# Kernel optimization log

Hardware: AMD Instinct MI355X
Metric: run time of the kernel (lower is better)

The kernel has to match this reference:

```python
import jax, jax.numpy as jnp
import numpy as np

EPS = 1e-5
K = 2  # superpatch hop


def _bn(x, gamma, beta, mean, var):
    # inference-mode BatchNorm2d over channel dim (NCHW)
    inv = gamma / jnp.sqrt(var + EPS)
    return x * inv[None, :, None, None] + (beta - mean * inv)[None, :, None, None]


def _conv1x1(x, w, b):
    # x: [B,C,H,W], w: [O,C], b: [O]
    return jnp.einsum('bchw,oc->bohw', x, w) + b[None, :, None, None]


def setup_inputs() -> dict:
    key = jax.random.key(0)
    ks = jax.random.split(key, 24)
    B, C, H, W = 32, 192, 56, 56
    r = lambda k, shape, s=0.05: jax.random.normal(k, shape, dtype=jnp.float32) * s
    pv = lambda k, shape: jax.random.uniform(k, shape, dtype=jnp.float32, minval=0.5, maxval=1.5)
    inp = {
        'x': jax.random.normal(ks[0], (B, C, H, W), dtype=jnp.float32),
        # RepCPE: depthwise 7x7 conv, groups=C -> weight [C,1,7,7]
        'cpe_w': r(ks[1], (C, 1, 7, 7)),
        'cpe_b': r(ks[2], (C,)),
        # fc1: 1x1 conv C->C + BN
        'fc1_w': r(ks[3], (C, C)), 'fc1_b': r(ks[4], (C,)),
        'bn1_g': pv(ks[5], (C,)), 'bn1_b': r(ks[6], (C,)),
        'bn1_m': r(ks[7], (C,), 0.1), 'bn1_v': pv(ks[8], (C,)),
        # graph_conv.nn: 1x1 conv 2C->C + BN + GELU
        'gc_w': r(ks[9], (C, 2 * C)), 'gc_b': r(ks[10], (C,)),
        'bng_g': pv(ks[11], (C,)), 'bng_b': r(ks[12], (C,)),
        'bng_m': r(ks[13], (C,), 0.1), 'bng_v': pv(ks[14], (C,)),
        # fc2: 1x1 conv C->C + BN
        'fc2_w': r(ks[15], (C, C)), 'fc2_b': r(ks[16], (C,)),
        'bn2_g': pv(ks[17], (C,)), 'bn2_b': r(ks[18], (C,)),
        'bn2_m': r(ks[19], (C,), 0.1), 'bn2_v': pv(ks[20], (C,)),
    }
    return inp


def reference(x, cpe_w, cpe_b, fc1_w, fc1_b, bn1_g, bn1_b, bn1_m, bn1_v,
              gc_w, gc_b, bng_g, bng_b, bng_m, bng_v,
              fc2_w, fc2_b, bn2_g, bn2_b, bn2_m, bn2_v):
    C = x.shape[1]
    # --- RepCPE: depthwise 7x7 conv + bias, residual add ---
    pe = jax.lax.conv_general_dilated(
        x, cpe_w, window_strides=(1, 1), padding='SAME',
        feature_group_count=C,
        dimension_numbers=('NCHW', 'OIHW', 'NCHW'))
    x = pe + cpe_b[None, :, None, None] + x
    # --- fc1: 1x1 conv + BN ---
    x = _bn(_conv1x1(x, fc1_w, fc1_b), bn1_g, bn1_b, bn1_m, bn1_v)
    # --- MRConv4d: max-relative over 4 shifted neighbor views ---
    # torch.cat([x[..., -K:, :], x[..., :-K, :]], dim=2) == roll(+K) along H, etc.
    d = jnp.maximum(jnp.roll(x, K, axis=2) - x, jnp.roll(x, -K, axis=2) - x)
    d = jnp.maximum(d, jnp.roll(x, K, axis=3) - x)
    x_j = jnp.maximum(jnp.maximum(d, jnp.roll(x, -K, axis=3) - x), 0.0)  # x_j init = x - x = 0
    xc = jnp.concatenate([x, x_j], axis=1)  # [B,2C,H,W]
    x = jax.nn.gelu(_bn(_conv1x1(xc, gc_w, gc_b), bng_g, bng_b, bng_m, bng_v),
                    approximate=False)
    # --- fc2: 1x1 conv + BN ---
    x = _bn(_conv1x1(x, fc2_w, fc2_b), bn2_g, bn2_b, bn2_m, bn2_v)
    return x
```

## Files before the change

kernel.cpp:

```cpp
#include <hip/hip_runtime.h>
#include <hip/hip_bf16.h>


#define CC   192
#define HW   3136
#define NB   32

using short8 = __attribute__((ext_vector_type(8))) short;
using f32x4  = __attribute__((ext_vector_type(4))) float;

__device__ __forceinline__ float bf2f(short s) {
  union { unsigned u; float f; } x; x.u = ((unsigned)(unsigned short)s) << 16; return x.f;
}
__device__ __forceinline__ short f2bf(float f) {
  __hip_bfloat16 h = __float2bfloat16(f);
  return *reinterpret_cast<short*>(&h);
}
__device__ __forceinline__ float geluf(float v) {
  return 0.5f * v * (1.0f + erff(v * 0.70710678118654752f));
}
__device__ __forceinline__ void gl2lds(const char* g, char* l) {
  __builtin_amdgcn_global_load_lds(
      (const __attribute__((address_space(1))) void*)g,
      (__attribute__((address_space(3))) void*)l, 16, 0, 0);
}

__global__ void __launch_bounds__(256) fold_kernel(
    const float* __restrict__ fc1_w, const float* __restrict__ fc1_b,
    const float* __restrict__ bn1_g, const float* __restrict__ bn1_b,
    const float* __restrict__ bn1_m, const float* __restrict__ bn1_v,
    const float* __restrict__ gc_w,  const float* __restrict__ gc_b,
    const float* __restrict__ bng_g, const float* __restrict__ bng_b,
    const float* __restrict__ bng_m, const float* __restrict__ bng_v,
    const float* __restrict__ fc2_w, const float* __restrict__ fc2_b,
    const float* __restrict__ bn2_g, const float* __restrict__ bn2_b,
    const float* __restrict__ bn2_m, const float* __restrict__ bn2_v,
    __hip_bfloat16* __restrict__ W1f, __hip_bfloat16* __restrict__ Wgf, __hip_bfloat16* __restrict__ W2f,
    float* __restrict__ b1f, float* __restrict__ bgf, float* __restrict__ b2f) {
  int gt = blockIdx.x * 256 + threadIdx.x;
  if (gt < 3 * CC) {
    int which = gt / CC, o = gt - which * CC;
    const float *G, *Bt, *M, *V, *Bi; float* dst;
    if (which == 0)      { G = bn1_g; Bt = bn1_b; M = bn1_m; V = bn1_v; Bi = fc1_b; dst = b1f; }
    else if (which == 1) { G = bng_g; Bt = bng_b; M = bng_m; V = bng_v; Bi = gc_b;  dst = bgf; }
    else                 { G = bn2_g; Bt = bn2_b; M = bn2_m; V = bn2_v; Bi = fc2_b; dst = b2f; }
    float inv = G[o] * rsqrtf(V[o] + 1e-5f);
    dst[o] = Bi[o] * inv + Bt[o] - M[o] * inv;
  }
  int i = gt;
  if (i < CC * CC) {
    int o = i / CC;
    float inv = bn1_g[o] * rsqrtf(bn1_v[o] + 1e-5f);
    W1f[i] = __float2bfloat16(fc1_w[i] * inv);
  } else if (i < CC * CC + CC * 2 * CC) {
    int j = i - CC * CC; int o = j / (2 * CC);
    float inv = bng_g[o] * rsqrtf(bng_v[o] + 1e-5f);
    Wgf[j] = __float2bfloat16(gc_w[j] * inv);
  } else if (i < CC * CC * 4) {
    int j = i - CC * CC * 3; int o = j / CC;
    float inv = bn2_g[o] * rsqrtf(bn2_v[o] + 1e-5f);
    W2f[j] = __float2bfloat16(fc2_w[j] * inv);
  }
}

#define CSTR 956
__global__ void __launch_bounds__(256, 4) dwconv_kernel(
    const float* __restrict__ x, const float* __restrict__ cw,
    const float* __restrict__ cb, __hip_bfloat16* __restrict__ y0pm) {
  __shared__ short in_t[16 * CSTR];
  const int t = threadIdx.x;
  int bb = blockIdx.x;
  const int rs = bb % 7;  bb /= 7;
  const int cg = bb % 12; bb /= 12;
  const int b  = bb;
  const int h0 = rs * 8;

  for (int i = t; i < 16 * CSTR / 8; i += 256) ((int4*)in_t)[i] = int4{0, 0, 0, 0};
  __syncthreads();

  for (int it = t; it < 16 * 14 * 14; it += 256) {
    int w4 = it % 14, rr = (it / 14) % 14, c = it / 196;
    int gh = h0 - 3 + rr;
    if (gh >= 0 && gh < 56) {
      float4 v = *(const float4*)(x + ((size_t)(b * CC + cg * 16 + c) * 56 + gh) * 56 + w4 * 4);
      short4 s4 = { f2bf(v.x), f2bf(v.y), f2bf(v.z), f2bf(v.w) };
      *(short4*)(in_t + c * CSTR + rr * 68 + 4 + w4 * 4) = s4;
    }
  }
  __syncthreads();

  const int c = t & 15, g = t >> 4;
  const int cgx = g % 7, rh = g / 7;
  if (g < 14) {
    const float* wp = cw + (cg * 16 + c) * 49;
    const float bias = cb[cg * 16 + c];
    const short* base = in_t + c * CSTR + rh * 4 * 68 + cgx * 8;
    float acc[4][8] = {};
    float wr[7], wn[7];
#pragma unroll
    for (int i = 0; i < 7; ++i) wr[i] = wp[i];
#pragma unroll
    for (int kh = 0; kh < 7; ++kh) {
      if (kh < 6) {
#pragma unroll
        for (int i = 0; i < 7; ++i) wn[i] = wp[(kh + 1) * 7 + i];
      }
      if (kh == 3) wr[3] += 1.0f;
#pragma unroll
      for (int r = 0; r < 4; ++r) {
        const short* rp = base + (r + kh) * 68;
        int2 q0 = *(const int2*)(rp);
        int2 q1 = *(const int2*)(rp + 4);
        int2 q2 = *(const int2*)(rp + 8);
        int2 q3 = *(const int2*)(rp + 12);
        int dw[8] = { q0.x, q0.y, q1.x, q1.y, q2.x, q2.y, q3.x, q3.y };
        float v[16];
#pragma unroll
        for (int q = 0; q < 8; ++q) {
          union { int i; float f; } lo, hi;
          lo.i = dw[q] << 16; hi.i = dw[q] & 0xffff0000;
          v[q * 2] = lo.f; v[q * 2 + 1] = hi.f;
        }
#pragma unroll
        for (int kw = 0; kw < 7; ++kw) {
          float wv = wr[kw];
#pragma unroll
          for (int ww = 0; ww < 8; ++ww)
            acc[r][ww] = fmaf(wv, v[ww + kw + 1], acc[r][ww]);
        }
      }
#pragma unroll
      for (int i = 0; i < 7; ++i) wr[i] = wn[i];
    }
    short* dst = (short*)y0pm + ((size_t)b * HW + (size_t)(h0 + rh * 4) * 56 + cgx * 8) * CC
                 + cg * 16 + c;
#pragma unroll
    for (int r = 0; r < 4; ++r)
#pragma unroll
      for (int ww = 0; ww < 8; ++ww)
        dst[(size_t)(r * 56 + ww) * CC] = f2bf(acc[r][ww] + bias);
  }
}

__device__ __forceinline__ void stage_xj(char* dst, const short* y1b, int hwbase, int t) {
#pragma unroll 2
  for (int j = 0; j < 6; ++j) {
    int idx = j * 4096 + t * 16;
    int p = idx / 384, qd = idx - p * 384;
    int co = qd >> 1;
    int hwl = hwbase + p;
    int h = hwl / 56, w = hwl - h * 56;
    int hp = (h >= 54) ? h - 54 : h + 2;
    int hm = (h < 2) ? h + 54 : h - 2;
    int wp_ = (w >= 54) ? w - 54 : w + 2;
    int wm_ = (w < 2) ? w + 54 : w - 2;
    short8 c0 = *(const short8*)(y1b + (size_t)hwl * CC + co);
    short8 n1 = *(const short8*)(y1b + (size_t)(hp * 56 + w) * CC + co);
    short8 n2 = *(const short8*)(y1b + (size_t)(hm * 56 + w) * CC + co);
    short8 n3 = *(const short8*)(y1b + (size_t)(h * 56 + wp_) * CC + co);
    short8 n4 = *(const short8*)(y1b + (size_t)(h * 56 + wm_) * CC + co);
    short8 res;
#pragma unroll
    for (int q = 0; q < 8; ++q) {
      float m = fmaxf(fmaxf(bf2f(n1[q]), bf2f(n2[q])), fmaxf(bf2f(n3[q]), bf2f(n4[q])));
      res[q] = f2bf(fmaxf(m - bf2f(c0[q]), 0.0f));
    }
    *(short8*)(dst + p * 384 + (qd ^ ((p & 7) << 4))) = res;
  }
}

template<int NCHUNK, int MODE, int MINW>
__global__ void __launch_bounds__(256, MINW) gemm_kernel(
    const __hip_bfloat16* __restrict__ actA, const __hip_bfloat16* __restrict__ actB,
    const __hip_bfloat16* __restrict__ Wf, const float* __restrict__ bfv,
    void* __restrict__ outp) {
  __shared__ char smem[2][24576];
  const int t = threadIdx.x;
  const int lane = t & 63, w = t >> 6;
  const int lrow = lane & 15, lhi = lane >> 4;
  constexpr int K_IN = NCHUNK * 192;
  constexpr int NT = NB * 49;

  int goff[6];
#pragma unroll
  for (int j = 0; j < 6; ++j) {
    int idx = j * 4096 + t * 16;
    int p = idx / 384, qd = idx - p * 384;
    goff[j] = p * 384 + (qd ^ ((p & 7) << 4));
  }

  float bw0[3];
  float bw2[3][4];
  if (MODE != 2) {
#pragma unroll
    for (int wi = 0; wi < 3; ++wi) bw0[wi] = bfv[w * 48 + wi * 16 + lrow];
  } else {
#pragma unroll
    for (int wi = 0; wi < 3; ++wi)
#pragma unroll
      for (int r = 0; r < 4; ++r) bw2[wi][r] = bfv[w * 48 + wi * 16 + lhi * 4 + r];
  }

  short8 wreg[NCHUNK][6][3];
#pragma unroll
  for (int c = 0; c < NCHUNK; ++c)
#pragma unroll
    for (int kk = 0; kk < 6; ++kk)
#pragma unroll
      for (int wi = 0; wi < 3; ++wi) {
        int o = w * 48 + wi * 16 + lrow;
        wreg[c][kk][wi] = *(const short8*)((const short*)Wf +
            (size_t)o * K_IN + c * 192 + kk * 32 + lhi * 8);
      }

  const int step = gridDim.x;
  int tile = blockIdx.x;
  {
    const char* src = (const char*)actA + (size_t)tile * 24576;
#pragma unroll
    for (int j = 0; j < 6; ++j)
      gl2lds(src + goff[j], smem[0] + j * 4096 + w * 1024);
  }
  __syncthreads();
  int cur = 0;

  while (tile < NT) {
    const int tnext = tile + step;
    const int bimg = tile / 49;
    const int hwbase = (tile - bimg * 49) * 64;
    const short* y1b = (const short*)actA + (size_t)bimg * HW * CC;
    f32x4 acc[4][3] = {};
#pragma unroll
    for (int c = 0; c < NCHUNK; ++c) {
      if (MODE == 3 && c == 0) {
        stage_xj(smem[cur ^ 1], y1b, hwbase, t);
      } else {
        const char* nsrc = nullptr;
        if (c + 1 < NCHUNK)      nsrc = (const char*)actB + (size_t)tile * 24576;
        else if (tnext < NT)     nsrc = (const char*)actA + (size_t)tnext * 24576;
        if (nsrc) {
#pragma unroll
          for (int j = 0; j < 6; ++j)
            gl2lds(nsrc + goff[j], smem[cur ^ 1] + j * 4096 + w * 1024);
        }
      }
#pragma unroll
      for (int kk = 0; kk < 6; ++kk) {
        short8 af[4];
#pragma unroll
        for (int ai = 0; ai < 4; ++ai) {
          int p = ai * 16 + lrow;
          af[ai] = *(const short8*)(smem[cur] + p * 384 + ((kk * 64 + lhi * 16) ^ ((p & 7) << 4)));
        }
#pragma unroll
        for (int ai = 0; ai < 4; ++ai)
#pragma unroll
          for (int wi = 0; wi < 3; ++wi)
            acc[ai][wi] = (MODE == 2)
                ? __builtin_amdgcn_mfma_f32_16x16x32_bf16(wreg[c][kk][wi], af[ai], acc[ai][wi], 0, 0, 0)
                : __builtin_amdgcn_mfma_f32_16x16x32_bf16(af[ai], wreg[c][kk][wi], acc[ai][wi], 0, 0, 0);
      }
      __syncthreads();
      cur ^= 1;
    }
    if (MODE != 2) {
      short* ob = (short*)outp + (size_t)tile * 64 * CC;
#pragma unroll
      for (int wi = 0; wi < 3; ++wi) {
        int o = w * 48 + wi * 16 + lrow;
#pragma unroll
        for (int ai = 0; ai < 4; ++ai)
#pragma unroll
          for (int r = 0; r < 4; ++r) {
            int p = ai * 16 + lhi * 4 + r;
            float v = acc[ai][wi][r] + bw0[wi];
            if (MODE == 3) v = geluf(v);
            ob[(size_t)p * CC + o] = f2bf(v);
          }
      }
    } else {
      float* ob = (float*)outp + (size_t)bimg * CC * HW + hwbase;
#pragma unroll
      for (int wi = 0; wi < 3; ++wi)
#pragma unroll
        for (int r = 0; r < 4; ++r) {
          int o = w * 48 + wi * 16 + lhi * 4 + r;
#pragma unroll
          for (int ai = 0; ai < 4; ++ai)
            ob[(size_t)o * HW + ai * 16 + lrow] = acc[ai][wi][r] + bw2[wi][r];
        }
    }
    tile = tnext;
  }
}

extern "C" void kernel_launch(void* const* d_in, const int* in_sizes, int n_in,
                              void* d_out, int out_size, void* d_ws, size_t ws_size,
                              hipStream_t stream) {
  const float* x     = (const float*)d_in[0];
  const float* cpe_w = (const float*)d_in[1];
  const float* cpe_b = (const float*)d_in[2];
  const float* fc1_w = (const float*)d_in[3];
  const float* fc1_b = (const float*)d_in[4];
  const float* bn1_g = (const float*)d_in[5];
  const float* bn1_b = (const float*)d_in[6];
  const float* bn1_m = (const float*)d_in[7];
  const float* bn1_v = (const float*)d_in[8];
  const float* gc_w  = (const float*)d_in[9];
  const float* gc_b  = (const float*)d_in[10];
  const float* bng_g = (const float*)d_in[11];
  const float* bng_b = (const float*)d_in[12];
  const float* bng_m = (const float*)d_in[13];
  const float* bng_v = (const float*)d_in[14];
  const float* fc2_w = (const float*)d_in[15];
  const float* fc2_b = (const float*)d_in[16];
  const float* bn2_g = (const float*)d_in[17];
  const float* bn2_b = (const float*)d_in[18];
  const float* bn2_m = (const float*)d_in[19];
  const float* bn2_v = (const float*)d_in[20];

  if (ws_size < 77594624) return;
  char* ws = (char*)d_ws;
  __hip_bfloat16* W1f = (__hip_bfloat16*)(ws);
  __hip_bfloat16* Wgf = (__hip_bfloat16*)(ws + 73728);
  __hip_bfloat16* W2f = (__hip_bfloat16*)(ws + 221184);
  float* b1f = (float*)(ws + 294912);
  float* bgf = (float*)(ws + 295680);
  float* b2f = (float*)(ws + 296448);
  __hip_bfloat16* y0  = (__hip_bfloat16*)(ws + 524288);
  __hip_bfloat16* y1  = (__hip_bfloat16*)d_out;
  float* out = (float*)d_out;

  fold_kernel<<<576, 256, 0, stream>>>(fc1_w, fc1_b, bn1_g, bn1_b, bn1_m, bn1_v,
      gc_w, gc_b, bng_g, bng_b, bng_m, bng_v, fc2_w, fc2_b, bn2_g, bn2_b, bn2_m, bn2_v,
      W1f, Wgf, W2f, b1f, bgf, b2f);
  dwconv_kernel<<<NB * 12 * 7, 256, 0, stream>>>(x, cpe_w, cpe_b, y0);
  gemm_kernel<1, 0, 2><<<512, 256, 0, stream>>>(y0, nullptr, W1f, b1f, y1);
  gemm_kernel<2, 3, 2><<<512, 256, 0, stream>>>(y1, nullptr, Wgf, bgf, y0);
  gemm_kernel<1, 2, 2><<<512, 256, 0, stream>>>(y0, nullptr, W2f, b2f, out);
}
```

Baseline: 163.1 us.

## Interleave max-relative staging with MFMA loop and use tanh GELU

The x_j neighbour gather, previously a separate staging pass before the chunk-0 MFMA loop, is now software-pipelined into the kk loop. Each iteration prefetches the next segment's five neighbour vectors while computing and writing the current one, so the gather loads overlap with the matrix math. Exact erf GELU is also replaced by a tanh approximation built on __expf, which is cheaper in the epilogue. The tradeoff is more register pressure from the extra short8 buffers and a small numerical deviation from exact GELU.

```diff
diff --git a/kernel.cpp b/kernel.cpp
--- a/kernel.cpp
+++ b/kernel.cpp
@@ -17,7 +17,9 @@
   return *reinterpret_cast<short*>(&h);
 }
 __device__ __forceinline__ float geluf(float v) {
-  return 0.5f * v * (1.0f + erff(v * 0.70710678118654752f));
+  float u = 0.7978845608028654f * (v + 0.044715f * v * v * v);
+  float e = __expf(2.0f * u);
+  return 0.5f * v * (2.0f - 2.0f / (e + 1.0f));
 }
 __device__ __forceinline__ void gl2lds(const char* g, char* l) {
   __builtin_amdgcn_global_load_lds(
@@ -142,31 +144,27 @@
   }
 }
 
-__device__ __forceinline__ void stage_xj(char* dst, const short* y1b, int hwbase, int t) {
-#pragma unroll 2
-  for (int j = 0; j < 6; ++j) {
-    int idx = j * 4096 + t * 16;
-    int p = idx / 384, qd = idx - p * 384;
-    int co = qd >> 1;
-    int hwl = hwbase + p;
-    int h = hwl / 56, w = hwl - h * 56;
-    int hp = (h >= 54) ? h - 54 : h + 2;
-    int hm = (h < 2) ? h + 54 : h - 2;
-    int wp_ = (w >= 54) ? w - 54 : w + 2;
-    int wm_ = (w < 2) ? w + 54 : w - 2;
-    short8 c0 = *(const short8*)(y1b + (size_t)hwl * CC + co);
-    short8 n1 = *(const short8*)(y1b + (size_t)(hp * 56 + w) * CC + co);
-    short8 n2 = *(const short8*)(y1b + (size_t)(hm * 56 + w) * CC + co);
-    short8 n3 = *(const short8*)(y1b + (size_t)(h * 56 + wp_) * CC + co);
-    short8 n4 = *(const short8*)(y1b + (size_t)(h * 56 + wm_) * CC + co);
-    short8 res;
-#pragma unroll
-    for (int q = 0; q < 8; ++q) {
-      float m = fmaxf(fmaxf(bf2f(n1[q]), bf2f(n2[q])), fmaxf(bf2f(n3[q]), bf2f(n4[q])));
-      res[q] = f2bf(fmaxf(m - bf2f(c0[q]), 0.0f));
-    }
-    *(short8*)(dst + p * 384 + (qd ^ ((p & 7) << 4))) = res;
-  }
+__device__ __forceinline__ void xj_load(short8 (&nb)[5], const short* y1c, int hwl) {
+  int h = hwl / 56, w = hwl - h * 56;
+  int hp = (h >= 54) ? h - 54 : h + 2;
+  int hm = (h < 2) ? h + 54 : h - 2;
+  int wp = (w >= 54) ? w - 54 : w + 2;
+  int wm = (w < 2) ? w + 54 : w - 2;
+  nb[0] = *(const short8*)(y1c + (size_t)hwl * CC);
+  nb[1] = *(const short8*)(y1c + (size_t)(hp * 56 + w) * CC);
+  nb[2] = *(const short8*)(y1c + (size_t)(hm * 56 + w) * CC);
+  nb[3] = *(const short8*)(y1c + (size_t)(h * 56 + wp) * CC);
+  nb[4] = *(const short8*)(y1c + (size_t)(h * 56 + wm) * CC);
+}
+__device__ __forceinline__ void xj_write(char* dst, const short8 (&nb)[5], int dstoff) {
+  short8 res;
+#pragma unroll
+  for (int q = 0; q < 8; ++q) {
+    float m = fmaxf(fmaxf(bf2f(nb[1][q]), bf2f(nb[2][q])),
+                    fmaxf(bf2f(nb[3][q]), bf2f(nb[4][q])));
+    res[q] = f2bf(fmaxf(m - bf2f(nb[0][q]), 0.0f));
+  }
+  *(short8*)(dst + dstoff) = res;
 }
 
 template<int NCHUNK, int MODE, int MINW>
@@ -181,12 +179,13 @@
   constexpr int K_IN = NCHUNK * 192;
   constexpr int NT = NB * 49;
 
-  int goff[6];
+  int sp[6], sq[6], goff[6];
 #pragma unroll
   for (int j = 0; j < 6; ++j) {
     int idx = j * 4096 + t * 16;
-    int p = idx / 384, qd = idx - p * 384;
-    goff[j] = p * 384 + (qd ^ ((p & 7) << 4));
+    sp[j] = idx / 384;
+    sq[j] = idx - sp[j] * 384;
+    goff[j] = sp[j] * 384 + (sq[j] ^ ((sp[j] & 7) << 4));
   }
 
   float bw0[3];
@@ -232,9 +231,7 @@
     f32x4 acc[4][3] = {};
 #pragma unroll
     for (int c = 0; c < NCHUNK; ++c) {
-      if (MODE == 3 && c == 0) {
-        stage_xj(smem[cur ^ 1], y1b, hwbase, t);
-      } else {
+      if (!(MODE == 3 && c == 0)) {
         const char* nsrc = nullptr;
         if (c + 1 < NCHUNK)      nsrc = (const char*)actB + (size_t)tile * 24576;
         else if (tnext < NT)     nsrc = (const char*)actA + (size_t)tnext * 24576;
@@ -244,8 +241,16 @@
             gl2lds(nsrc + goff[j], smem[cur ^ 1] + j * 4096 + w * 1024);
         }
       }
+      short8 nb[5];
+      if (MODE == 3 && c == 0)
+        xj_load(nb, y1b + (sq[0] >> 1), hwbase + sp[0]);
 #pragma unroll
       for (int kk = 0; kk < 6; ++kk) {
+        short8 nb2[5];
+        if (MODE == 3 && c == 0) {
+          if (kk < 5) xj_load(nb2, y1b + (sq[kk + 1] >> 1), hwbase + sp[kk + 1]);
+          xj_write(smem[cur ^ 1], nb, goff[kk]);
+        }
         short8 af[4];
 #pragma unroll
         for (int ai = 0; ai < 4; ++ai) {
@@ -259,6 +264,10 @@
             acc[ai][wi] = (MODE == 2)
                 ? __builtin_amdgcn_mfma_f32_16x16x32_bf16(wreg[c][kk][wi], af[ai], acc[ai][wi], 0, 0, 0)
                 : __builtin_amdgcn_mfma_f32_16x16x32_bf16(af[ai], wreg[c][kk][wi], acc[ai][wi], 0, 0, 0);
+        if (MODE == 3 && c == 0 && kk < 5) {
+#pragma unroll
+          for (int q = 0; q < 5; ++q) nb[q] = nb2[q];
+        }
       }
       __syncthreads();
       cur ^= 1;
```

Result: slower. 186.0 us (+14.0%).
